# Performance work log

Measured on AMD Instinct MI355X. Metric: run time of the kernel, lower is better.

The kernel has to match this reference:

```python
import jax, jax.numpy as jnp
import numpy as np
import math

N_NODES = 100000
N_EDGES = 1600000
D_FEAT = 32
K = 1        # Bernstein index k
N_ORD = 2    # Bernstein order n
COMB = float(math.comb(N_ORD, K))


def setup_inputs() -> dict:
    key = jax.random.key(0)
    k1, k2, k3 = jax.random.split(key, 3)
    feat = jax.random.normal(k1, (N_NODES, D_FEAT), dtype=jnp.float32)
    edge_src = jax.random.randint(k2, (N_EDGES,), 0, N_NODES)
    edge_dst = jax.random.randint(k3, (N_EDGES,), 0, N_NODES)
    return {"feat": feat, "edge_src": edge_src, "edge_dst": edge_dst}


def reference(feat, edge_src, edge_dst):
    # in-degree of each node (copy_u/sum aggregates over incoming edges)
    deg = jax.ops.segment_sum(jnp.ones((N_EDGES,), feat.dtype), edge_dst,
                              num_segments=N_NODES)
    d_invsqrt = jnp.clip(deg, 1.0, None) ** -0.5  # [N]
    d_invsqrt = d_invsqrt[:, None]                 # [N,1]

    def unn_laplacian(x):
        msg = (x * d_invsqrt)[edge_src]            # [E,D]
        agg = jax.ops.segment_sum(msg, edge_dst, num_segments=N_NODES)
        return x - agg * d_invsqrt

    if K == 0:
        h = feat
        for _ in range(N_ORD):
            h = unn_laplacian(h) / 2
            h = feat - h
    elif K == N_ORD:
        h = feat
        for _ in range(N_ORD):
            h = unn_laplacian(h) / 2
    else:
        temp = feat
        for _ in range(K):
            temp = unn_laplacian(temp) / 2
        h = feat
        for _ in range(N_ORD - K):
            h = unn_laplacian(h) / 2
            h = feat - h
        h = temp * h
    return COMB * h
```

## Files before the change

### kernel.cpp

```cpp
#include <hip/hip_runtime.h>

#define N_NODES 100000
#define N_EDGES 1600000
#define D_FEAT 32

#define BSH 7
#define BMASK 127
#define NB 782
#define CAPB 2432

#define P1_BS 512
#define P1_TILE 4096
#define P1_CAP 16


typedef float v4f __attribute__((ext_vector_type(4)));

static __device__ __forceinline__ unsigned pack_bf16(float a, float b) {
    unsigned ua = __float_as_uint(a);
    unsigned ub = __float_as_uint(b);
    ua = (ua + 0x7FFFu + ((ua >> 16) & 1u)) >> 16;
    ub = (ub + 0x7FFFu + ((ub >> 16) & 1u)) >> 16;
    return (ua & 0xFFFFu) | (ub << 16);
}

__global__ void init_kernel(int* __restrict__ cursorA) {
    int b = blockIdx.x * blockDim.x + threadIdx.x;
    if (b < NB) cursorA[b] = b * CAPB;
}

__global__ void __launch_bounds__(P1_BS)
bucket_kernel(const int* __restrict__ edge_src,
              const int* __restrict__ edge_dst,
              int* __restrict__ cursorA,
              int* __restrict__ pairs, int n_edges) {
    __shared__ int s_cnt[NB];
    __shared__ int s_base[NB];
    __shared__ int s_buf[NB * P1_CAP];

    int tile = blockIdx.x * P1_TILE;
    if (tile >= n_edges) return;

    for (int b = threadIdx.x; b < NB; b += P1_BS) s_cnt[b] = 0;
    __syncthreads();

    const int4* src4 = reinterpret_cast<const int4*>(edge_src);
    const int4* dst4 = reinterpret_cast<const int4*>(edge_dst);
    int tileq = blockIdx.x * (P1_TILE / 4);
    #pragma unroll
    for (int j = 0; j < P1_TILE / 4 / P1_BS; ++j) {
        int iq = tileq + j * P1_BS + threadIdx.x;
        if (iq * 4 < n_edges) {
            int4 sv = src4[iq];
            int4 dv = dst4[iq];
            int ss[4] = {sv.x, sv.y, sv.z, sv.w};
            int dd[4] = {dv.x, dv.y, dv.z, dv.w};
            #pragma unroll
            for (int u = 0; u < 4; ++u) {
                int b = dd[u] >> BSH;
                int packed = (ss[u] << BSH) | (dd[u] & BMASK);
                int p = atomicAdd(&s_cnt[b], 1);
                if (p < P1_CAP) {
                    s_buf[b * P1_CAP + p] = packed;
                } else {
                    int gp = atomicAdd(&cursorA[b], 1);
                    pairs[gp] = packed;
                }
            }
        }
    }
    __syncthreads();

    for (int b = threadIdx.x; b < NB; b += P1_BS) {
        int c = min(s_cnt[b], P1_CAP);
        s_cnt[b] = c;
        s_base[b] = atomicAdd(&cursorA[b], c);
    }
    __syncthreads();

    for (int idx = threadIdx.x; idx < NB * P1_CAP; idx += P1_BS) {
        int b = idx >> 4;
        int slot = idx & (P1_CAP - 1);
        if (slot < s_cnt[b])
            pairs[s_base[b] + slot] = s_buf[idx];
    }
}

__global__ void __launch_bounds__(256)
sort_kernel(const int* __restrict__ pairs,
            const int* __restrict__ cursorA,
            const float* __restrict__ feat,
            int* __restrict__ ssrc,
            int2* __restrict__ srange,
            float* __restrict__ dinv,
            unsigned* __restrict__ sfeat) {
    __shared__ int buf[CAPB];
    __shared__ int outb[CAPB];
    __shared__ int h[128];
    __shared__ int sc[128];
    __shared__ int cur[128];
    __shared__ float dv_s[128];

    int b = blockIdx.x;
    int t = threadIdx.x;
    int base = b * CAPB;
    int cnt = min(cursorA[b] - base, CAPB);

    if (t < 128) h[t] = 0;
    __syncthreads();
    for (int i = t; i < cnt; i += 256) {
        int p = pairs[base + i];
        buf[i] = p;
        atomicAdd(&h[p & BMASK], 1);
    }
    __syncthreads();

    int v = 0;
    if (t < 128) { v = h[t]; sc[t] = v; }
    __syncthreads();
    for (int off = 1; off < 128; off <<= 1) {
        int x = 0;
        if (t < 128 && t >= off) x = sc[t - off];
        __syncthreads();
        if (t < 128) sc[t] += x;
        __syncthreads();
    }
    if (t < 128) {
        int ex = sc[t] - v;
        cur[t] = ex;
        int node = (b << BSH) + t;
        if (node < N_NODES) {
            srange[node] = make_int2(base + ex, base + ex + v);
            float dvv = rsqrtf(fmaxf((float)v, 1.0f));
            dinv[node] = dvv;
            dv_s[t] = dvv;
        }
    }
    __syncthreads();

    for (int i = t; i < cnt; i += 256) {
        int p = buf[i];
        int pos = atomicAdd(&cur[p & BMASK], 1);
        outb[pos] = p >> BSH;
    }
    __syncthreads();
    for (int i = t; i < cnt; i += 256)
        ssrc[base + i] = outb[i];

    const float4* feat4 = reinterpret_cast<const float4*>(feat);
    uint4* sf4 = reinterpret_cast<uint4*>(sfeat);
    for (int idx = t; idx < 128 * 4; idx += 256) {
        int nl = idx >> 2;
        int q = idx & 3;
        int node = (b << BSH) + nl;
        if (node >= N_NODES) continue;
        float dvv = dv_s[nl];
        float4 fa = feat4[node * 8 + 2 * q];
        float4 fb = feat4[node * 8 + 2 * q + 1];
        uint4 pk;
        pk.x = pack_bf16(fa.x * dvv, fa.y * dvv);
        pk.y = pack_bf16(fa.z * dvv, fa.w * dvv);
        pk.z = pack_bf16(fb.x * dvv, fb.y * dvv);
        pk.w = pack_bf16(fb.z * dvv, fb.w * dvv);
        sf4[node * 4 + q] = pk;
    }
}

__global__ void gather_bf_kernel(const float* __restrict__ feat,
                                 const unsigned* __restrict__ sfeat,
                                 const int2* __restrict__ srange,
                                 const int* __restrict__ ssrc,
                                 const float* __restrict__ dinv,
                                 float* __restrict__ out) {
    int gid = blockIdx.x * blockDim.x + threadIdx.x;
    int node = gid >> 2;
    int q = gid & 3;
    if (node >= N_NODES) return;
    int2 se = srange[node];
    int k = se.x, en = se.y;
    const uint4* sf4 = reinterpret_cast<const uint4*>(sfeat);
    float a0 = 0.f, a1 = 0.f, a2 = 0.f, a3 = 0.f;
    float a4 = 0.f, a5 = 0.f, a6 = 0.f, a7 = 0.f;

    #define ACC(r)                                                 \
        a0 += __uint_as_float((r).x << 16);                        \
        a1 += __uint_as_float((r).x & 0xFFFF0000u);                \
        a2 += __uint_as_float((r).y << 16);                        \
        a3 += __uint_as_float((r).y & 0xFFFF0000u);                \
        a4 += __uint_as_float((r).z << 16);                        \
        a5 += __uint_as_float((r).z & 0xFFFF0000u);                \
        a6 += __uint_as_float((r).w << 16);                        \
        a7 += __uint_as_float((r).w & 0xFFFF0000u);

    for (; k + 7 < en; k += 8) {
        int s0 = ssrc[k],     s1 = ssrc[k + 1];
        int s2 = ssrc[k + 2], s3 = ssrc[k + 3];
        int s4 = ssrc[k + 4], s5 = ssrc[k + 5];
        int s6 = ssrc[k + 6], s7 = ssrc[k + 7];
        uint4 r0 = sf4[s0 * 4 + q];
        uint4 r1 = sf4[s1 * 4 + q];
        uint4 r2 = sf4[s2 * 4 + q];
        uint4 r3 = sf4[s3 * 4 + q];
        uint4 r4 = sf4[s4 * 4 + q];
        uint4 r5 = sf4[s5 * 4 + q];
        uint4 r6 = sf4[s6 * 4 + q];
        uint4 r7 = sf4[s7 * 4 + q];
        ACC(r0) ACC(r1) ACC(r2) ACC(r3)
        ACC(r4) ACC(r5) ACC(r6) ACC(r7)
    }
    for (; k + 3 < en; k += 4) {
        int s0 = ssrc[k],     s1 = ssrc[k + 1];
        int s2 = ssrc[k + 2], s3 = ssrc[k + 3];
        uint4 r0 = sf4[s0 * 4 + q];
        uint4 r1 = sf4[s1 * 4 + q];
        uint4 r2 = sf4[s2 * 4 + q];
        uint4 r3 = sf4[s3 * 4 + q];
        ACC(r0) ACC(r1) ACC(r2) ACC(r3)
    }
    for (; k < en; ++k) {
        uint4 r = sf4[ssrc[k] * 4 + q];
        ACC(r)
    }
    #undef ACC

    float dvn = dinv[node];
    const v4f* featv = reinterpret_cast<const v4f*>(feat);
    v4f fa = __builtin_nontemporal_load(&featv[node * 8 + 2 * q]);
    v4f fb = __builtin_nontemporal_load(&featv[node * 8 + 2 * q + 1]);
    v4f oa, ob;
    float y;
    y = 0.5f * (fa.x - a0 * dvn); oa.x = 2.0f * y * (fa.x - y);
    y = 0.5f * (fa.y - a1 * dvn); oa.y = 2.0f * y * (fa.y - y);
    y = 0.5f * (fa.z - a2 * dvn); oa.z = 2.0f * y * (fa.z - y);
    y = 0.5f * (fa.w - a3 * dvn); oa.w = 2.0f * y * (fa.w - y);
    y = 0.5f * (fb.x - a4 * dvn); ob.x = 2.0f * y * (fb.x - y);
    y = 0.5f * (fb.y - a5 * dvn); ob.y = 2.0f * y * (fb.y - y);
    y = 0.5f * (fb.z - a6 * dvn); ob.z = 2.0f * y * (fb.z - y);
    y = 0.5f * (fb.w - a7 * dvn); ob.w = 2.0f * y * (fb.w - y);
    v4f* outv = reinterpret_cast<v4f*>(out);
    __builtin_nontemporal_store(oa, &outv[node * 8 + 2 * q]);
    __builtin_nontemporal_store(ob, &outv[node * 8 + 2 * q + 1]);
}

extern "C" void kernel_launch(void* const* d_in, const int* in_sizes, int n_in,
                              void* d_out, int out_size, void* d_ws, size_t ws_size,
                              hipStream_t stream) {
    const float* feat = (const float*)d_in[0];
    const int* edge_src = (const int*)d_in[1];
    const int* edge_dst = (const int*)d_in[2];
    float* out = (float*)d_out;

    int* ws = (int*)d_ws;
    int* cursorA   = ws;
    int2* srange   = (int2*)(cursorA + 1024);
    float* dinv    = (float*)(srange + N_NODES);
    int* ssrc      = (int*)(dinv + N_NODES);
    int* pairs     = ssrc + NB * CAPB;
    unsigned* sfeat = (unsigned*)(pairs + NB * CAPB);

    init_kernel<<<1, 1024, 0, stream>>>(cursorA);
    {
        int blocks = (N_EDGES + P1_TILE - 1) / P1_TILE;
        bucket_kernel<<<blocks, P1_BS, 0, stream>>>(edge_src, edge_dst,
                                                    cursorA, pairs, N_EDGES);
    }
    sort_kernel<<<NB, 256, 0, stream>>>(pairs, cursorA, feat, ssrc, srange,
                                        dinv, sfeat);
    {
        int total = N_NODES * 4;
        int blocks = (total + 255) / 256;
        gather_bf_kernel<<<blocks, 256, 0, stream>>>(feat, sfeat, srange,
                                                     ssrc, dinv, out);
    }
}
```

Baseline: 119.9 us.

## Replace per-bucket counting sort with shared-memory atomic accumulation in gather

Drops the intra-bucket counting sort (scan, scatter, ssrc/srange writes). The gather now runs one block per 128-node bucket, reads the unsorted (src,dst) pairs directly and accumulates bf16-decoded features into a padded shared-memory float array using LDS float atomics, then applies the epilogue per node. This removes a sort pass and its global traffic, but replaces register accumulation with many LDS atomic adds (8 per edge per thread), which may contend on hot rows. Float summation order also becomes nondeterministic.

```diff
diff --git a/kernel.cpp b/kernel.cpp
--- a/kernel.cpp
+++ b/kernel.cpp
@@ -12,6 +12,8 @@
 #define P1_BS 512
 #define P1_TILE 4096
 #define P1_CAP 16
+
+#define ACCW 33
 
 
 typedef float v4f __attribute__((ext_vector_type(4)));
@@ -87,18 +89,12 @@
 }
 
 __global__ void __launch_bounds__(256)
-sort_kernel(const int* __restrict__ pairs,
+prep_kernel(const int* __restrict__ pairs,
             const int* __restrict__ cursorA,
             const float* __restrict__ feat,
-            int* __restrict__ ssrc,
-            int2* __restrict__ srange,
             float* __restrict__ dinv,
             unsigned* __restrict__ sfeat) {
-    __shared__ int buf[CAPB];
-    __shared__ int outb[CAPB];
     __shared__ int h[128];
-    __shared__ int sc[128];
-    __shared__ int cur[128];
     __shared__ float dv_s[128];
 
     int b = blockIdx.x;
@@ -108,44 +104,19 @@
 
     if (t < 128) h[t] = 0;
     __syncthreads();
-    for (int i = t; i < cnt; i += 256) {
-        int p = pairs[base + i];
-        buf[i] = p;
-        atomicAdd(&h[p & BMASK], 1);
-    }
-    __syncthreads();
-
-    int v = 0;
-    if (t < 128) { v = h[t]; sc[t] = v; }
-    __syncthreads();
-    for (int off = 1; off < 128; off <<= 1) {
-        int x = 0;
-        if (t < 128 && t >= off) x = sc[t - off];
-        __syncthreads();
-        if (t < 128) sc[t] += x;
-        __syncthreads();
-    }
+    for (int i = t; i < cnt; i += 256)
+        atomicAdd(&h[pairs[base + i] & BMASK], 1);
+    __syncthreads();
+
     if (t < 128) {
-        int ex = sc[t] - v;
-        cur[t] = ex;
         int node = (b << BSH) + t;
         if (node < N_NODES) {
-            srange[node] = make_int2(base + ex, base + ex + v);
-            float dvv = rsqrtf(fmaxf((float)v, 1.0f));
+            float dvv = rsqrtf(fmaxf((float)h[t], 1.0f));
             dinv[node] = dvv;
             dv_s[t] = dvv;
         }
     }
     __syncthreads();
-
-    for (int i = t; i < cnt; i += 256) {
-        int p = buf[i];
-        int pos = atomicAdd(&cur[p & BMASK], 1);
-        outb[pos] = p >> BSH;
-    }
-    __syncthreads();
-    for (int i = t; i < cnt; i += 256)
-        ssrc[base + i] = outb[i];
 
     const float4* feat4 = reinterpret_cast<const float4*>(feat);
     uint4* sf4 = reinterpret_cast<uint4*>(sfeat);
@@ -166,80 +137,81 @@
     }
 }
 
-__global__ void gather_bf_kernel(const float* __restrict__ feat,
-                                 const unsigned* __restrict__ sfeat,
-                                 const int2* __restrict__ srange,
-                                 const int* __restrict__ ssrc,
-                                 const float* __restrict__ dinv,
-                                 float* __restrict__ out) {
-    int gid = blockIdx.x * blockDim.x + threadIdx.x;
-    int node = gid >> 2;
-    int q = gid & 3;
-    if (node >= N_NODES) return;
-    int2 se = srange[node];
-    int k = se.x, en = se.y;
+__global__ void __launch_bounds__(256)
+gather_acc_kernel(const int* __restrict__ pairs,
+                  const int* __restrict__ cursorA,
+                  const float* __restrict__ feat,
+                  const unsigned* __restrict__ sfeat,
+                  const float* __restrict__ dinv,
+                  float* __restrict__ out) {
+    __shared__ float acc[128 * ACCW];
+
+    int b = blockIdx.x;
+    int t = threadIdx.x;
+    int base = b * CAPB;
+    int cnt = min(cursorA[b] - base, CAPB);
+
+    for (int i = t; i < 128 * ACCW; i += 256) acc[i] = 0.f;
+    __syncthreads();
+
+    int q = t & 3;
+    int eg = t >> 2;
     const uint4* sf4 = reinterpret_cast<const uint4*>(sfeat);
-    float a0 = 0.f, a1 = 0.f, a2 = 0.f, a3 = 0.f;
-    float a4 = 0.f, a5 = 0.f, a6 = 0.f, a7 = 0.f;
-
-    #define ACC(r)                                                 \
-        a0 += __uint_as_float((r).x << 16);                        \
-        a1 += __uint_as_float((r).x & 0xFFFF0000u);                \
-        a2 += __uint_as_float((r).y << 16);                        \
-        a3 += __uint_as_float((r).y & 0xFFFF0000u);                \
-        a4 += __uint_as_float((r).z << 16);                        \
-        a5 += __uint_as_float((r).z & 0xFFFF0000u);                \
-        a6 += __uint_as_float((r).w << 16);                        \
-        a7 += __uint_as_float((r).w & 0xFFFF0000u);
-
-    for (; k + 7 < en; k += 8) {
-        int s0 = ssrc[k],     s1 = ssrc[k + 1];
-        int s2 = ssrc[k + 2], s3 = ssrc[k + 3];
-        int s4 = ssrc[k + 4], s5 = ssrc[k + 5];
-        int s6 = ssrc[k + 6], s7 = ssrc[k + 7];
-        uint4 r0 = sf4[s0 * 4 + q];
-        uint4 r1 = sf4[s1 * 4 + q];
-        uint4 r2 = sf4[s2 * 4 + q];
-        uint4 r3 = sf4[s3 * 4 + q];
-        uint4 r4 = sf4[s4 * 4 + q];
-        uint4 r5 = sf4[s5 * 4 + q];
-        uint4 r6 = sf4[s6 * 4 + q];
-        uint4 r7 = sf4[s7 * 4 + q];
-        ACC(r0) ACC(r1) ACC(r2) ACC(r3)
-        ACC(r4) ACC(r5) ACC(r6) ACC(r7)
-    }
-    for (; k + 3 < en; k += 4) {
-        int s0 = ssrc[k],     s1 = ssrc[k + 1];
-        int s2 = ssrc[k + 2], s3 = ssrc[k + 3];
-        uint4 r0 = sf4[s0 * 4 + q];
-        uint4 r1 = sf4[s1 * 4 + q];
-        uint4 r2 = sf4[s2 * 4 + q];
-        uint4 r3 = sf4[s3 * 4 + q];
-        ACC(r0) ACC(r1) ACC(r2) ACC(r3)
-    }
-    for (; k < en; ++k) {
-        uint4 r = sf4[ssrc[k] * 4 + q];
-        ACC(r)
-    }
-    #undef ACC
-
-    float dvn = dinv[node];
+
+    #define ADD8(aptr, r)                                                  \
+        unsafeAtomicAdd((aptr) + 0, __uint_as_float((r).x << 16));         \
+        unsafeAtomicAdd((aptr) + 1, __uint_as_float((r).x & 0xFFFF0000u)); \
+        unsafeAtomicAdd((aptr) + 2, __uint_as_float((r).y << 16));         \
+        unsafeAtomicAdd((aptr) + 3, __uint_as_float((r).y & 0xFFFF0000u)); \
+        unsafeAtomicAdd((aptr) + 4, __uint_as_float((r).z << 16));         \
+        unsafeAtomicAdd((aptr) + 5, __uint_as_float((r).z & 0xFFFF0000u)); \
+        unsafeAtomicAdd((aptr) + 6, __uint_as_float((r).w << 16));         \
+        unsafeAtomicAdd((aptr) + 7, __uint_as_float((r).w & 0xFFFF0000u));
+
+    int e = eg;
+    for (; e + 64 < cnt; e += 128) {
+        int p0 = pairs[base + e];
+        int p1 = pairs[base + e + 64];
+        uint4 r0 = sf4[(p0 >> BSH) * 4 + q];
+        uint4 r1 = sf4[(p1 >> BSH) * 4 + q];
+        float* a0 = &acc[(p0 & BMASK) * ACCW + q * 8];
+        float* a1 = &acc[(p1 & BMASK) * ACCW + q * 8];
+        ADD8(a0, r0)
+        ADD8(a1, r1)
+    }
+    for (; e < cnt; e += 64) {
+        int p0 = pairs[base + e];
+        uint4 r0 = sf4[(p0 >> BSH) * 4 + q];
+        float* a0 = &acc[(p0 & BMASK) * ACCW + q * 8];
+        ADD8(a0, r0)
+    }
+    #undef ADD8
+    __syncthreads();
+
     const v4f* featv = reinterpret_cast<const v4f*>(feat);
-    v4f fa = __builtin_nontemporal_load(&featv[node * 8 + 2 * q]);
-    v4f fb = __builtin_nontemporal_load(&featv[node * 8 + 2 * q + 1]);
-    v4f oa, ob;
-    float y;
-    y = 0.5f * (fa.x - a0 * dvn); oa.x = 2.0f * y * (fa.x - y);
-    y = 0.5f * (fa.y - a1 * dvn); oa.y = 2.0f * y * (fa.y - y);
-    y = 0.5f * (fa.z - a2 * dvn); oa.z = 2.0f * y * (fa.z - y);
-    y = 0.5f * (fa.w - a3 * dvn); oa.w = 2.0f * y * (fa.w - y);
-    y = 0.5f * (fb.x - a4 * dvn); ob.x = 2.0f * y * (fb.x - y);
-    y = 0.5f * (fb.y - a5 * dvn); ob.y = 2.0f * y * (fb.y - y);
-    y = 0.5f * (fb.z - a6 * dvn); ob.z = 2.0f * y * (fb.z - y);
-    y = 0.5f * (fb.w - a7 * dvn); ob.w = 2.0f * y * (fb.w - y);
     v4f* outv = reinterpret_cast<v4f*>(out);
-    __builtin_nontemporal_store(oa, &outv[node * 8 + 2 * q]);
-    __builtin_nontemporal_store(ob, &outv[node * 8 + 2 * q + 1]);
+    for (int idx = t; idx < 128 * 4; idx += 256) {
+        int nl = idx >> 2;
+        int qq = idx & 3;
+        int node = (b << BSH) + nl;
+        if (node >= N_NODES) continue;
+        float dvn = dinv[node];
+        const float* a = &acc[nl * ACCW + qq * 8];
+        v4f fa = __builtin_nontemporal_load(&featv[node * 8 + 2 * qq]);
+        v4f fb = __builtin_nontemporal_load(&featv[node * 8 + 2 * qq + 1]);
+        v4f oa, ob;
+        float y;
+        y = 0.5f * (fa.x - a[0] * dvn); oa.x = 2.0f * y * (fa.x - y);
+        y = 0.5f * (fa.y - a[1] * dvn); oa.y = 2.0f * y * (fa.y - y);
+        y = 0.5f * (fa.z - a[2] * dvn); oa.z = 2.0f * y * (fa.z - y);
+        y = 0.5f * (fa.w - a[3] * dvn); oa.w = 2.0f * y * (fa.w - y);
+        y = 0.5f * (fb.x - a[4] * dvn); ob.x = 2.0f * y * (fb.x - y);
+        y = 0.5f * (fb.y - a[5] * dvn); ob.y = 2.0f * y * (fb.y - y);
+        y = 0.5f * (fb.z - a[6] * dvn); ob.z = 2.0f * y * (fb.z - y);
+        y = 0.5f * (fb.w - a[7] * dvn); ob.w = 2.0f * y * (fb.w - y);
+        __builtin_nontemporal_store(oa, &outv[node * 8 + 2 * qq]);
+        __builtin_nontemporal_store(ob, &outv[node * 8 + 2 * qq + 1]);
+    }
 }
 
 extern "C" void kernel_launch(void* const* d_in, const int* in_sizes, int n_in,
@@ -251,11 +223,9 @@
     float* out = (float*)d_out;
 
     int* ws = (int*)d_ws;
-    int* cursorA   = ws;
-    int2* srange   = (int2*)(cursorA + 1024);
-    float* dinv    = (float*)(srange + N_NODES);
-    int* ssrc      = (int*)(dinv + N_NODES);
-    int* pairs     = ssrc + NB * CAPB;
+    int* cursorA    = ws;
+    float* dinv     = (float*)(cursorA + 1024);
+    int* pairs      = (int*)(dinv + N_NODES);
     unsigned* sfeat = (unsigned*)(pairs + NB * CAPB);
 
     init_kernel<<<1, 1024, 0, stream>>>(cursorA);
@@ -264,12 +234,7 @@
         bucket_kernel<<<blocks, P1_BS, 0, stream>>>(edge_src, edge_dst,
                                                     cursorA, pairs, N_EDGES);
     }
-    sort_kernel<<<NB, 256, 0, stream>>>(pairs, cursorA, feat, ssrc, srange,
-                                        dinv, sfeat);
-    {
-        int total = N_NODES * 4;
-        int blocks = (total + 255) / 256;
-        gather_bf_kernel<<<blocks, 256, 0, stream>>>(feat, sfeat, srange,
-                                                     ssrc, dinv, out);
-    }
-}
+    prep_kernel<<<NB, 256, 0, stream>>>(pairs, cursorA, feat, dinv, sfeat);
+    gather_acc_kernel<<<NB, 256, 0, stream>>>(pairs, cursorA, feat, sfeat,
+                                              dinv, out);
+}
```

Measured after the change: 429.5 us. 258% more time.

## Fuse bucket sort into gather kernel, keeping sorted sources in shared memory

Applied to the files above, without the earlier changes.

Splits the old sort kernel. A light prep kernel now only computes degrees and writes the scaled bf16 features. A new fused kernel redoes the per-bucket counting sort in shared memory and gathers directly from the LDS-resident source list, so the global ssrc, srange and dinv arrays are no longer written and re-read. The cost is that the histogram is computed twice, and the gather now runs with only 782 blocks of 256 threads covering 128 nodes each, which lowers parallelism and occupancy for the latency-bound gather. Shared-memory usage per block is about 20KB, which may also limit occupancy.

```diff
diff --git a/kernel.cpp b/kernel.cpp
--- a/kernel.cpp
+++ b/kernel.cpp
@@ -87,18 +87,11 @@
 }
 
 __global__ void __launch_bounds__(256)
-sort_kernel(const int* __restrict__ pairs,
+prep_kernel(const int* __restrict__ pairs,
             const int* __restrict__ cursorA,
             const float* __restrict__ feat,
-            int* __restrict__ ssrc,
-            int2* __restrict__ srange,
-            float* __restrict__ dinv,
             unsigned* __restrict__ sfeat) {
-    __shared__ int buf[CAPB];
-    __shared__ int outb[CAPB];
     __shared__ int h[128];
-    __shared__ int sc[128];
-    __shared__ int cur[128];
     __shared__ float dv_s[128];
 
     int b = blockIdx.x;
@@ -108,44 +101,13 @@
 
     if (t < 128) h[t] = 0;
     __syncthreads();
-    for (int i = t; i < cnt; i += 256) {
-        int p = pairs[base + i];
-        buf[i] = p;
-        atomicAdd(&h[p & BMASK], 1);
-    }
-    __syncthreads();
-
-    int v = 0;
-    if (t < 128) { v = h[t]; sc[t] = v; }
-    __syncthreads();
-    for (int off = 1; off < 128; off <<= 1) {
-        int x = 0;
-        if (t < 128 && t >= off) x = sc[t - off];
-        __syncthreads();
-        if (t < 128) sc[t] += x;
-        __syncthreads();
-    }
-    if (t < 128) {
-        int ex = sc[t] - v;
-        cur[t] = ex;
-        int node = (b << BSH) + t;
-        if (node < N_NODES) {
-            srange[node] = make_int2(base + ex, base + ex + v);
-            float dvv = rsqrtf(fmaxf((float)v, 1.0f));
-            dinv[node] = dvv;
-            dv_s[t] = dvv;
-        }
-    }
-    __syncthreads();
-
-    for (int i = t; i < cnt; i += 256) {
-        int p = buf[i];
-        int pos = atomicAdd(&cur[p & BMASK], 1);
-        outb[pos] = p >> BSH;
-    }
-    __syncthreads();
     for (int i = t; i < cnt; i += 256)
-        ssrc[base + i] = outb[i];
+        atomicAdd(&h[pairs[base + i] & BMASK], 1);
+    __syncthreads();
+
+    if (t < 128)
+        dv_s[t] = rsqrtf(fmaxf((float)h[t], 1.0f));
+    __syncthreads();
 
     const float4* feat4 = reinterpret_cast<const float4*>(feat);
     uint4* sf4 = reinterpret_cast<uint4*>(sfeat);
@@ -166,80 +128,127 @@
     }
 }
 
-__global__ void gather_bf_kernel(const float* __restrict__ feat,
-                                 const unsigned* __restrict__ sfeat,
-                                 const int2* __restrict__ srange,
-                                 const int* __restrict__ ssrc,
-                                 const float* __restrict__ dinv,
-                                 float* __restrict__ out) {
-    int gid = blockIdx.x * blockDim.x + threadIdx.x;
-    int node = gid >> 2;
-    int q = gid & 3;
-    if (node >= N_NODES) return;
-    int2 se = srange[node];
-    int k = se.x, en = se.y;
+__global__ void __launch_bounds__(256)
+sortgather_kernel(const int* __restrict__ pairs,
+                  const int* __restrict__ cursorA,
+                  const float* __restrict__ feat,
+                  const unsigned* __restrict__ sfeat,
+                  float* __restrict__ out) {
+    __shared__ int buf[CAPB];
+    __shared__ int outb[CAPB];
+    __shared__ int h[128];
+    __shared__ int sc[128];
+    __shared__ int cur[128];
+    __shared__ float dv_s[128];
+
+    int b = blockIdx.x;
+    int t = threadIdx.x;
+    int base = b * CAPB;
+    int cnt = min(cursorA[b] - base, CAPB);
+
+    if (t < 128) h[t] = 0;
+    __syncthreads();
+    for (int i = t; i < cnt; i += 256) {
+        int p = pairs[base + i];
+        buf[i] = p;
+        atomicAdd(&h[p & BMASK], 1);
+    }
+    __syncthreads();
+
+    int v = 0;
+    if (t < 128) { v = h[t]; sc[t] = v; }
+    __syncthreads();
+    for (int off = 1; off < 128; off <<= 1) {
+        int x = 0;
+        if (t < 128 && t >= off) x = sc[t - off];
+        __syncthreads();
+        if (t < 128) sc[t] += x;
+        __syncthreads();
+    }
+    if (t < 128) {
+        cur[t] = sc[t] - v;
+        dv_s[t] = rsqrtf(fmaxf((float)v, 1.0f));
+    }
+    __syncthreads();
+
+    for (int i = t; i < cnt; i += 256) {
+        int p = buf[i];
+        int pos = atomicAdd(&cur[p & BMASK], 1);
+        outb[pos] = p >> BSH;
+    }
+    __syncthreads();
+
     const uint4* sf4 = reinterpret_cast<const uint4*>(sfeat);
-    float a0 = 0.f, a1 = 0.f, a2 = 0.f, a3 = 0.f;
-    float a4 = 0.f, a5 = 0.f, a6 = 0.f, a7 = 0.f;
-
-    #define ACC(r)                                                 \
-        a0 += __uint_as_float((r).x << 16);                        \
-        a1 += __uint_as_float((r).x & 0xFFFF0000u);                \
-        a2 += __uint_as_float((r).y << 16);                        \
-        a3 += __uint_as_float((r).y & 0xFFFF0000u);                \
-        a4 += __uint_as_float((r).z << 16);                        \
-        a5 += __uint_as_float((r).z & 0xFFFF0000u);                \
-        a6 += __uint_as_float((r).w << 16);                        \
-        a7 += __uint_as_float((r).w & 0xFFFF0000u);
-
-    for (; k + 7 < en; k += 8) {
-        int s0 = ssrc[k],     s1 = ssrc[k + 1];
-        int s2 = ssrc[k + 2], s3 = ssrc[k + 3];
-        int s4 = ssrc[k + 4], s5 = ssrc[k + 5];
-        int s6 = ssrc[k + 6], s7 = ssrc[k + 7];
-        uint4 r0 = sf4[s0 * 4 + q];
-        uint4 r1 = sf4[s1 * 4 + q];
-        uint4 r2 = sf4[s2 * 4 + q];
-        uint4 r3 = sf4[s3 * 4 + q];
-        uint4 r4 = sf4[s4 * 4 + q];
-        uint4 r5 = sf4[s5 * 4 + q];
-        uint4 r6 = sf4[s6 * 4 + q];
-        uint4 r7 = sf4[s7 * 4 + q];
-        ACC(r0) ACC(r1) ACC(r2) ACC(r3)
-        ACC(r4) ACC(r5) ACC(r6) ACC(r7)
-    }
-    for (; k + 3 < en; k += 4) {
-        int s0 = ssrc[k],     s1 = ssrc[k + 1];
-        int s2 = ssrc[k + 2], s3 = ssrc[k + 3];
-        uint4 r0 = sf4[s0 * 4 + q];
-        uint4 r1 = sf4[s1 * 4 + q];
-        uint4 r2 = sf4[s2 * 4 + q];
-        uint4 r3 = sf4[s3 * 4 + q];
-        ACC(r0) ACC(r1) ACC(r2) ACC(r3)
-    }
-    for (; k < en; ++k) {
-        uint4 r = sf4[ssrc[k] * 4 + q];
-        ACC(r)
-    }
-    #undef ACC
-
-    float dvn = dinv[node];
     const v4f* featv = reinterpret_cast<const v4f*>(feat);
-    v4f fa = __builtin_nontemporal_load(&featv[node * 8 + 2 * q]);
-    v4f fb = __builtin_nontemporal_load(&featv[node * 8 + 2 * q + 1]);
-    v4f oa, ob;
-    float y;
-    y = 0.5f * (fa.x - a0 * dvn); oa.x = 2.0f * y * (fa.x - y);
-    y = 0.5f * (fa.y - a1 * dvn); oa.y = 2.0f * y * (fa.y - y);
-    y = 0.5f * (fa.z - a2 * dvn); oa.z = 2.0f * y * (fa.z - y);
-    y = 0.5f * (fa.w - a3 * dvn); oa.w = 2.0f * y * (fa.w - y);
-    y = 0.5f * (fb.x - a4 * dvn); ob.x = 2.0f * y * (fb.x - y);
-    y = 0.5f * (fb.y - a5 * dvn); ob.y = 2.0f * y * (fb.y - y);
-    y = 0.5f * (fb.z - a6 * dvn); ob.z = 2.0f * y * (fb.z - y);
-    y = 0.5f * (fb.w - a7 * dvn); ob.w = 2.0f * y * (fb.w - y);
     v4f* outv = reinterpret_cast<v4f*>(out);
-    __builtin_nontemporal_store(oa, &outv[node * 8 + 2 * q]);
-    __builtin_nontemporal_store(ob, &outv[node * 8 + 2 * q + 1]);
+
+    for (int item = t; item < 128 * 4; item += 256) {
+        int nl = item >> 2;
+        int q = item & 3;
+        int node = (b << BSH) + nl;
+        if (node >= N_NODES) continue;
+        int en = sc[nl];
+        int k = en - h[nl];
+        float a0 = 0.f, a1 = 0.f, a2 = 0.f, a3 = 0.f;
+        float a4 = 0.f, a5 = 0.f, a6 = 0.f, a7 = 0.f;
+
+        #define ACC(r)                                                 \
+            a0 += __uint_as_float((r).x << 16);                        \
+            a1 += __uint_as_float((r).x & 0xFFFF0000u);                \
+            a2 += __uint_as_float((r).y << 16);                        \
+            a3 += __uint_as_float((r).y & 0xFFFF0000u);                \
+            a4 += __uint_as_float((r).z << 16);                        \
+            a5 += __uint_as_float((r).z & 0xFFFF0000u);                \
+            a6 += __uint_as_float((r).w << 16);                        \
+            a7 += __uint_as_float((r).w & 0xFFFF0000u);
+
+        for (; k + 7 < en; k += 8) {
+            int s0 = outb[k],     s1 = outb[k + 1];
+            int s2 = outb[k + 2], s3 = outb[k + 3];
+            int s4 = outb[k + 4], s5 = outb[k + 5];
+            int s6 = outb[k + 6], s7 = outb[k + 7];
+            uint4 r0 = sf4[s0 * 4 + q];
+            uint4 r1 = sf4[s1 * 4 + q];
+            uint4 r2 = sf4[s2 * 4 + q];
+            uint4 r3 = sf4[s3 * 4 + q];
+            uint4 r4 = sf4[s4 * 4 + q];
+            uint4 r5 = sf4[s5 * 4 + q];
+            uint4 r6 = sf4[s6 * 4 + q];
+            uint4 r7 = sf4[s7 * 4 + q];
+            ACC(r0) ACC(r1) ACC(r2) ACC(r3)
+            ACC(r4) ACC(r5) ACC(r6) ACC(r7)
+        }
+        for (; k + 3 < en; k += 4) {
+            int s0 = outb[k],     s1 = outb[k + 1];
+            int s2 = outb[k + 2], s3 = outb[k + 3];
+            uint4 r0 = sf4[s0 * 4 + q];
+            uint4 r1 = sf4[s1 * 4 + q];
+            uint4 r2 = sf4[s2 * 4 + q];
+            uint4 r3 = sf4[s3 * 4 + q];
+            ACC(r0) ACC(r1) ACC(r2) ACC(r3)
+        }
+        for (; k < en; ++k) {
+            uint4 r = sf4[outb[k] * 4 + q];
+            ACC(r)
+        }
+        #undef ACC
+
+        float dvn = dv_s[nl];
+        v4f fa = __builtin_nontemporal_load(&featv[node * 8 + 2 * q]);
+        v4f fb = __builtin_nontemporal_load(&featv[node * 8 + 2 * q + 1]);
+        v4f oa, ob;
+        float y;
+        y = 0.5f * (fa.x - a0 * dvn); oa.x = 2.0f * y * (fa.x - y);
+        y = 0.5f * (fa.y - a1 * dvn); oa.y = 2.0f * y * (fa.y - y);
+        y = 0.5f * (fa.z - a2 * dvn); oa.z = 2.0f * y * (fa.z - y);
+        y = 0.5f * (fa.w - a3 * dvn); oa.w = 2.0f * y * (fa.w - y);
+        y = 0.5f * (fb.x - a4 * dvn); ob.x = 2.0f * y * (fb.x - y);
+        y = 0.5f * (fb.y - a5 * dvn); ob.y = 2.0f * y * (fb.y - y);
+        y = 0.5f * (fb.z - a6 * dvn); ob.z = 2.0f * y * (fb.z - y);
+        y = 0.5f * (fb.w - a7 * dvn); ob.w = 2.0f * y * (fb.w - y);
+        __builtin_nontemporal_store(oa, &outv[node * 8 + 2 * q]);
+        __builtin_nontemporal_store(ob, &outv[node * 8 + 2 * q + 1]);
+    }
 }
 
 extern "C" void kernel_launch(void* const* d_in, const int* in_sizes, int n_in,
@@ -251,11 +260,8 @@
     float* out = (float*)d_out;
 
     int* ws = (int*)d_ws;
-    int* cursorA   = ws;
-    int2* srange   = (int2*)(cursorA + 1024);
-    float* dinv    = (float*)(srange + N_NODES);
-    int* ssrc      = (int*)(dinv + N_NODES);
-    int* pairs     = ssrc + NB * CAPB;
+    int* cursorA    = ws;
+    int* pairs      = cursorA + 1024;
     unsigned* sfeat = (unsigned*)(pairs + NB * CAPB);
 
     init_kernel<<<1, 1024, 0, stream>>>(cursorA);
@@ -264,12 +270,6 @@
         bucket_kernel<<<blocks, P1_BS, 0, stream>>>(edge_src, edge_dst,
                                                     cursorA, pairs, N_EDGES);
     }
-    sort_kernel<<<NB, 256, 0, stream>>>(pairs, cursorA, feat, ssrc, srange,
-                                        dinv, sfeat);
-    {
-        int total = N_NODES * 4;
-        int blocks = (total + 255) / 256;
-        gather_bf_kernel<<<blocks, 256, 0, stream>>>(feat, sfeat, srange,
-                                                     ssrc, dinv, out);
-    }
-}
+    prep_kernel<<<NB, 256, 0, stream>>>(pairs, cursorA, feat, sfeat);
+    sortgather_kernel<<<NB, 256, 0, stream>>>(pairs, cursorA, feat, sfeat, out);
+}
```

After: 117.5 us. 2.0% less time.
